# Optimization experiments

Measured on AMD Instinct MI355X. Metric: run time of the kernel, lower is better.

## Reference

```python
import jax, jax.numpy as jnp
import numpy as np

N_NODES = 100000


def _gcn_layer(x, W, b, src, dst, edge_weight):
    # GCNConv with normalize=False: linear transform, then weighted scatter-add
    h = x @ W                                   # [N, out]
    msg = h[src] * edge_weight[:, None]         # gather source features, scale per edge
    agg = jax.ops.segment_sum(msg, dst, num_segments=N_NODES)  # scatter-add to destinations
    return agg + b


def setup_inputs() -> dict:
    key = jax.random.key(0)
    k = jax.random.split(key, 6)
    N, F_in, H, C, E = N_NODES, 256, 16, 40, 3200000
    x = jax.random.normal(k[0], (N, F_in), dtype=jnp.float32)
    edge_index = jax.random.randint(k[1], (2, E), 0, N, dtype=jnp.int64)
    edge_weight = jax.random.uniform(k[2], (E,), dtype=jnp.float32)
    # Glorot-style init for weights
    W1 = jax.random.normal(k[3], (F_in, H), dtype=jnp.float32) * (1.0 / np.sqrt(F_in))
    b1 = jnp.zeros((H,), dtype=jnp.float32)
    W2 = jax.random.normal(k[4], (H, C), dtype=jnp.float32) * (1.0 / np.sqrt(H))
    b2 = jnp.zeros((C,), dtype=jnp.float32)
    return {"x": x, "edge_index": edge_index, "edge_weight": edge_weight,
            "W1": W1, "b1": b1, "W2": W2, "b2": b2}


def reference(x, edge_index, edge_weight, W1, b1, W2, b2):
    src, dst = edge_index[0], edge_index[1]
    h = jax.nn.relu(_gcn_layer(x, W1, b1, src, dst, edge_weight))
    # dropout is identity in eval mode
    h = _gcn_layer(h, W2, b2, src, dst, edge_weight)
    return jax.nn.log_softmax(h, axis=1)
```

## Files before the change

### kernel.cpp

```cpp
#include <hip/hip_runtime.h>
#include <hip/hip_bf16.h>
#include <cstdint>

#define F_IN 256
#define F_H  16
#define F_P  8
#define F_C  40

__global__ __launch_bounds__(256) void gemm1_kernel(
    const float* __restrict__ x, const float* __restrict__ W1,
    __hip_bfloat162* __restrict__ t1, int N) {
  __shared__ float wlds[F_IN * F_H];
  __shared__ float xlds[16 * 260];
  const int tid = threadIdx.x;
  const int nodeBase = blockIdx.x * 16;

  for (int i = tid; i < F_IN * F_H; i += 256) wlds[i] = W1[i];

  const float4* x4 = reinterpret_cast<const float4*>(x) + (size_t)nodeBase * (F_IN / 4);
  for (int i = tid; i < 16 * (F_IN / 4); i += 256) {
    int r = i >> 6;
    int c4 = i & 63;
    float4 v = make_float4(0.f, 0.f, 0.f, 0.f);
    if (nodeBase + r < N) v = x4[(size_t)r * (F_IN / 4) + c4];
    *reinterpret_cast<float4*>(&xlds[r * 260 + c4 * 4]) = v;
  }
  __syncthreads();

  const int r = tid >> 4;
  const int f = tid & 15;
  const float* xr = &xlds[r * 260];
  float acc = 0.f;
#pragma unroll 8
  for (int k = 0; k < F_IN; ++k) acc = fmaf(xr[k], wlds[k * F_H + f], acc);

  float hi = __shfl_down(acc, 1);
  if (((f & 1) == 0) && (nodeBase + r < N)) {
    __hip_bfloat162 h2 = __halves2bfloat162(__float2bfloat16(acc), __float2bfloat16(hi));
    t1[(size_t)(nodeBase + r) * F_P + (f >> 1)] = h2;
  }
}

__global__ __launch_bounds__(256) void scatter1_kernel(
    const __hip_bfloat162* __restrict__ t1, const int* __restrict__ ei,
    const float* __restrict__ ew, __hip_bfloat162* __restrict__ agg1,
    int N, int E) {
  int gid = blockIdx.x * 256 + threadIdx.x;
  int e = gid >> 3;
  int p = gid & 7;
  if (e >= E) return;
  int s = ei[e];
  int d = ei[E + e];
  if ((unsigned)s >= (unsigned)N || (unsigned)d >= (unsigned)N) return;
  float w = ew[e];
  __hip_bfloat162 tv = t1[(size_t)s * F_P + p];
  __hip_bfloat162 v = __halves2bfloat162(
      __float2bfloat16(__bfloat162float(tv.x) * w),
      __float2bfloat16(__bfloat162float(tv.y) * w));
  unsafeAtomicAdd(&agg1[(size_t)d * F_P + p], v);
}

__global__ __launch_bounds__(256) void scatter2_kernel(
    const __hip_bfloat162* __restrict__ agg1, const float* __restrict__ b1,
    const int* __restrict__ ei, const float* __restrict__ ew,
    __hip_bfloat162* __restrict__ agg2, int N, int E) {
  int gid = blockIdx.x * 256 + threadIdx.x;
  int e = gid >> 3;
  int p = gid & 7;
  if (e >= E) return;
  int s = ei[e];
  int d = ei[E + e];
  if ((unsigned)s >= (unsigned)N || (unsigned)d >= (unsigned)N) return;
  float w = ew[e];
  __hip_bfloat162 av = agg1[(size_t)s * F_P + p];
  float lo = __bfloat162float(av.x) + b1[2 * p];
  float hi = __bfloat162float(av.y) + b1[2 * p + 1];
  lo = lo > 0.f ? lo * w : 0.f;
  hi = hi > 0.f ? hi * w : 0.f;
  __hip_bfloat162 v = __halves2bfloat162(__float2bfloat16(lo), __float2bfloat16(hi));
  unsafeAtomicAdd(&agg2[(size_t)d * F_P + p], v);
}

__global__ __launch_bounds__(320) void gemm2_lsm_kernel(
    const __hip_bfloat162* __restrict__ agg2, const float* __restrict__ W2,
    const float* __restrict__ b2, float* __restrict__ out, int N) {
  __shared__ float w2lds[F_H * F_C];
  __shared__ float alds[8 * F_H];
  __shared__ float slds[8 * F_C];
  __shared__ float mlog[8];
  const int tid = threadIdx.x;
  const int nodeBase = blockIdx.x * 8;

  for (int i = tid; i < F_H * F_C; i += 320) w2lds[i] = W2[i];
  if (tid < 8 * F_P) {
    int node = nodeBase + (tid >> 3);
    __hip_bfloat162 v{};
    if (node < N) v = agg2[(size_t)nodeBase * F_P + tid];
    int r = tid >> 3, p = tid & 7;
    alds[r * F_H + 2 * p]     = __bfloat162float(v.x);
    alds[r * F_H + 2 * p + 1] = __bfloat162float(v.y);
  }
  __syncthreads();

  const int ln = tid / F_C;
  const int c = tid - ln * F_C;
  float acc = b2[c];
#pragma unroll
  for (int k = 0; k < F_H; ++k) acc = fmaf(alds[ln * F_H + k], w2lds[k * F_C + c], acc);
  slds[tid] = acc;
  __syncthreads();

  if (tid < 8) {
    const float* row = &slds[tid * F_C];
    float m = -INFINITY;
#pragma unroll
    for (int f = 0; f < F_C; ++f) m = fmaxf(m, row[f]);
    float s = 0.f;
#pragma unroll
    for (int f = 0; f < F_C; ++f) s += expf(row[f] - m);
    mlog[tid] = m + logf(s);
  }
  __syncthreads();

  const int node = nodeBase + ln;
  if (node < N) out[(size_t)nodeBase * F_C + tid] = slds[tid] - mlog[ln];
}

extern "C" void kernel_launch(void* const* d_in, const int* in_sizes, int n_in,
                              void* d_out, int out_size, void* d_ws, size_t ws_size,
                              hipStream_t stream) {
  const float* x  = (const float*)d_in[0];
  const int*   ei = (const int*)d_in[1];
  const float* ew = (const float*)d_in[2];
  const float* W1 = (const float*)d_in[3];
  const float* b1 = (const float*)d_in[4];
  const float* W2 = (const float*)d_in[5];
  const float* b2 = (const float*)d_in[6];
  float* out = (float*)d_out;

  const int N = in_sizes[0] / F_IN;
  const int E = in_sizes[2];

  __hip_bfloat162* t1   = (__hip_bfloat162*)d_ws;
  __hip_bfloat162* agg1 = t1 + (size_t)N * F_P;
  __hip_bfloat162* agg2 = agg1 + (size_t)N * F_P;

  hipMemsetAsync(agg1, 0, (size_t)N * F_P * 2 * sizeof(__hip_bfloat162), stream);

  gemm1_kernel<<<(N + 15) / 16, 256, 0, stream>>>(x, W1, t1, N);
  scatter1_kernel<<<((size_t)E * F_P + 255) / 256, 256, 0, stream>>>(t1, ei, ew, agg1, N, E);
  scatter2_kernel<<<((size_t)E * F_P + 255) / 256, 256, 0, stream>>>(agg1, b1, ei, ew, agg2, N, E);
  gemm2_lsm_kernel<<<(N + 7) / 8, 320, 0, stream>>>(agg2, W2, b2, out, N);
}
```

Measured before the change: 552.9 us.

## Split atomic targets, fuse zeroing into persistent GEMM1, shuffle-based log-softmax

GEMM1 becomes a persistent grid-stride kernel that reads x straight from global memory, processes four nodes per thread against a transposed W1 held in LDS, and zeroes the aggregation buffers itself, which removes the separate memset. Both scatters send edges to two accumulator copies by edge parity, meant to halve atomic contention per address; consumers add the two copies back together. GEMM2 handles 32 nodes per block, each thread computing 5 classes, and does the log-softmax reduction with width-8 shuffles and fast exp/log in place of LDS passes and extra barriers. This costs twice the accumulator memory, an extra gather per edge in scatter2, and uncoalesced x reads in GEMM1.

```diff
diff --git a/kernel.cpp b/kernel.cpp
--- a/kernel.cpp
+++ b/kernel.cpp
@@ -6,45 +6,84 @@
 #define F_H  16
 #define F_P  8
 #define F_C  40
+#define GB   512
+#define XS   32
 
 __global__ __launch_bounds__(256) void gemm1_kernel(
     const float* __restrict__ x, const float* __restrict__ W1,
-    __hip_bfloat162* __restrict__ t1, int N) {
-  __shared__ float wlds[F_IN * F_H];
-  __shared__ float xlds[16 * 260];
+    unsigned* __restrict__ t1, uint4* __restrict__ aggz, int N) {
+  __shared__ float wlds[F_H * 260];
   const int tid = threadIdx.x;
-  const int nodeBase = blockIdx.x * 16;
-
-  for (int i = tid; i < F_IN * F_H; i += 256) wlds[i] = W1[i];
-
-  const float4* x4 = reinterpret_cast<const float4*>(x) + (size_t)nodeBase * (F_IN / 4);
-  for (int i = tid; i < 16 * (F_IN / 4); i += 256) {
-    int r = i >> 6;
-    int c4 = i & 63;
-    float4 v = make_float4(0.f, 0.f, 0.f, 0.f);
-    if (nodeBase + r < N) v = x4[(size_t)r * (F_IN / 4) + c4];
-    *reinterpret_cast<float4*>(&xlds[r * 260 + c4 * 4]) = v;
+
+  {
+    const size_t tot = (size_t)N * F_P;
+    for (size_t i = blockIdx.x * 256 + tid; i < tot; i += (size_t)GB * 256)
+      aggz[i] = make_uint4(0u, 0u, 0u, 0u);
+  }
+
+  for (int i = tid; i < F_IN * F_H; i += 256) {
+    int k = i >> 4, f = i & 15;
+    wlds[f * 260 + k] = W1[i];
   }
   __syncthreads();
 
-  const int r = tid >> 4;
-  const int f = tid & 15;
-  const float* xr = &xlds[r * 260];
-  float acc = 0.f;
+  const int lane = tid & 63;
+  const int wv   = tid >> 6;
+  const int f    = lane & 15;
+  const int qs   = lane >> 4;
+  const float4* wf4 = reinterpret_cast<const float4*>(&wlds[f * 260]);
+  const float4* x4  = reinterpret_cast<const float4*>(x);
+
+  for (int nb = blockIdx.x * 64 + wv * 16 + qs * 4; nb < N; nb += GB * 64) {
+    int n0 = nb, n1 = nb + 1, n2 = nb + 2, n3 = nb + 3;
+    int c1 = n1 < N ? n1 : N - 1;
+    int c2 = n2 < N ? n2 : N - 1;
+    int c3 = n3 < N ? n3 : N - 1;
+    const float4* xr0 = x4 + (size_t)n0 * 64;
+    const float4* xr1 = x4 + (size_t)c1 * 64;
+    const float4* xr2 = x4 + (size_t)c2 * 64;
+    const float4* xr3 = x4 + (size_t)c3 * 64;
+    float a0 = 0.f, a1 = 0.f, a2 = 0.f, a3 = 0.f;
 #pragma unroll 8
-  for (int k = 0; k < F_IN; ++k) acc = fmaf(xr[k], wlds[k * F_H + f], acc);
-
-  float hi = __shfl_down(acc, 1);
-  if (((f & 1) == 0) && (nodeBase + r < N)) {
-    __hip_bfloat162 h2 = __halves2bfloat162(__float2bfloat16(acc), __float2bfloat16(hi));
-    t1[(size_t)(nodeBase + r) * F_P + (f >> 1)] = h2;
+    for (int k4 = 0; k4 < 64; ++k4) {
+      float4 w = wf4[k4];
+      float4 v0 = xr0[k4], v1 = xr1[k4], v2 = xr2[k4], v3 = xr3[k4];
+      a0 = fmaf(v0.x, w.x, a0); a0 = fmaf(v0.y, w.y, a0);
+      a0 = fmaf(v0.z, w.z, a0); a0 = fmaf(v0.w, w.w, a0);
+      a1 = fmaf(v1.x, w.x, a1); a1 = fmaf(v1.y, w.y, a1);
+      a1 = fmaf(v1.z, w.z, a1); a1 = fmaf(v1.w, w.w, a1);
+      a2 = fmaf(v2.x, w.x, a2); a2 = fmaf(v2.y, w.y, a2);
+      a2 = fmaf(v2.z, w.z, a2); a2 = fmaf(v2.w, w.w, a2);
+      a3 = fmaf(v3.x, w.x, a3); a3 = fmaf(v3.y, w.y, a3);
+      a3 = fmaf(v3.z, w.z, a3); a3 = fmaf(v3.w, w.w, a3);
+    }
+    float p0 = __shfl_xor(a0, 1), p1 = __shfl_xor(a1, 1);
+    float p2 = __shfl_xor(a2, 1), p3 = __shfl_xor(a3, 1);
+    if ((f & 1) == 0) {
+      int pp = f >> 1;
+      __hip_bfloat162 h;
+      h = __halves2bfloat162(__float2bfloat16(a0), __float2bfloat16(p0));
+      t1[(size_t)n0 * F_P + pp] = *reinterpret_cast<unsigned*>(&h);
+      if (n1 < N) {
+        h = __halves2bfloat162(__float2bfloat16(a1), __float2bfloat16(p1));
+        t1[(size_t)n1 * F_P + pp] = *reinterpret_cast<unsigned*>(&h);
+      }
+      if (n2 < N) {
+        h = __halves2bfloat162(__float2bfloat16(a2), __float2bfloat16(p2));
+        t1[(size_t)n2 * F_P + pp] = *reinterpret_cast<unsigned*>(&h);
+      }
+      if (n3 < N) {
+        h = __halves2bfloat162(__float2bfloat16(a3), __float2bfloat16(p3));
+        t1[(size_t)n3 * F_P + pp] = *reinterpret_cast<unsigned*>(&h);
+      }
+    }
   }
 }
 
 __global__ __launch_bounds__(256) void scatter1_kernel(
     const __hip_bfloat162* __restrict__ t1, const int* __restrict__ ei,
-    const float* __restrict__ ew, __hip_bfloat162* __restrict__ agg1,
-    int N, int E) {
+    const float* __restrict__ ew, __hip_bfloat162* __restrict__ agg1a,
+    __hip_bfloat162* __restrict__ agg1b, int N, int E) {
   int gid = blockIdx.x * 256 + threadIdx.x;
   int e = gid >> 3;
   int p = gid & 7;
@@ -57,13 +96,16 @@
   __hip_bfloat162 v = __halves2bfloat162(
       __float2bfloat16(__bfloat162float(tv.x) * w),
       __float2bfloat16(__bfloat162float(tv.y) * w));
-  unsafeAtomicAdd(&agg1[(size_t)d * F_P + p], v);
+  __hip_bfloat162* tgt = (e & 1) ? agg1b : agg1a;
+  unsafeAtomicAdd(&tgt[(size_t)d * F_P + p], v);
 }
 
 __global__ __launch_bounds__(256) void scatter2_kernel(
-    const __hip_bfloat162* __restrict__ agg1, const float* __restrict__ b1,
+    const __hip_bfloat162* __restrict__ agg1a,
+    const __hip_bfloat162* __restrict__ agg1b, const float* __restrict__ b1,
     const int* __restrict__ ei, const float* __restrict__ ew,
-    __hip_bfloat162* __restrict__ agg2, int N, int E) {
+    __hip_bfloat162* __restrict__ agg2a, __hip_bfloat162* __restrict__ agg2b,
+    int N, int E) {
   int gid = blockIdx.x * 256 + threadIdx.x;
   int e = gid >> 3;
   int p = gid & 7;
@@ -72,58 +114,76 @@
   int d = ei[E + e];
   if ((unsigned)s >= (unsigned)N || (unsigned)d >= (unsigned)N) return;
   float w = ew[e];
-  __hip_bfloat162 av = agg1[(size_t)s * F_P + p];
-  float lo = __bfloat162float(av.x) + b1[2 * p];
-  float hi = __bfloat162float(av.y) + b1[2 * p + 1];
-  lo = lo > 0.f ? lo * w : 0.f;
-  hi = hi > 0.f ? hi * w : 0.f;
+  float2 bb = reinterpret_cast<const float2*>(b1)[p];
+  __hip_bfloat162 va = agg1a[(size_t)s * F_P + p];
+  __hip_bfloat162 vb = agg1b[(size_t)s * F_P + p];
+  float lo = fmaxf(__bfloat162float(va.x) + __bfloat162float(vb.x) + bb.x, 0.f) * w;
+  float hi = fmaxf(__bfloat162float(va.y) + __bfloat162float(vb.y) + bb.y, 0.f) * w;
   __hip_bfloat162 v = __halves2bfloat162(__float2bfloat16(lo), __float2bfloat16(hi));
-  unsafeAtomicAdd(&agg2[(size_t)d * F_P + p], v);
-}
-
-__global__ __launch_bounds__(320) void gemm2_lsm_kernel(
-    const __hip_bfloat162* __restrict__ agg2, const float* __restrict__ W2,
+  __hip_bfloat162* tgt = (e & 1) ? agg2b : agg2a;
+  unsafeAtomicAdd(&tgt[(size_t)d * F_P + p], v);
+}
+
+__global__ __launch_bounds__(256) void gemm2_lsm_kernel(
+    const __hip_bfloat162* __restrict__ agg2a,
+    const __hip_bfloat162* __restrict__ agg2b, const float* __restrict__ W2,
     const float* __restrict__ b2, float* __restrict__ out, int N) {
   __shared__ float w2lds[F_H * F_C];
-  __shared__ float alds[8 * F_H];
-  __shared__ float slds[8 * F_C];
-  __shared__ float mlog[8];
+  __shared__ float b2lds[F_C];
+  __shared__ float alds[XS * F_H];
   const int tid = threadIdx.x;
-  const int nodeBase = blockIdx.x * 8;
-
-  for (int i = tid; i < F_H * F_C; i += 320) w2lds[i] = W2[i];
-  if (tid < 8 * F_P) {
+  const int nodeBase = blockIdx.x * XS;
+
+  for (int i = tid; i < F_H * F_C; i += 256) w2lds[i] = W2[i];
+  if (tid < F_C) b2lds[tid] = b2[tid];
+  {
     int node = nodeBase + (tid >> 3);
-    __hip_bfloat162 v{};
-    if (node < N) v = agg2[(size_t)nodeBase * F_P + tid];
-    int r = tid >> 3, p = tid & 7;
-    alds[r * F_H + 2 * p]     = __bfloat162float(v.x);
-    alds[r * F_H + 2 * p + 1] = __bfloat162float(v.y);
+    float lo = 0.f, hi = 0.f;
+    if (node < N) {
+      size_t idx = (size_t)node * F_P + (tid & 7);
+      __hip_bfloat162 va = agg2a[idx];
+      __hip_bfloat162 vb = agg2b[idx];
+      lo = __bfloat162float(va.x) + __bfloat162float(vb.x);
+      hi = __bfloat162float(va.y) + __bfloat162float(vb.y);
+    }
+    alds[(tid >> 3) * F_H + 2 * (tid & 7)]     = lo;
+    alds[(tid >> 3) * F_H + 2 * (tid & 7) + 1] = hi;
   }
   __syncthreads();
 
-  const int ln = tid / F_C;
-  const int c = tid - ln * F_C;
-  float acc = b2[c];
-#pragma unroll
-  for (int k = 0; k < F_H; ++k) acc = fmaf(alds[ln * F_H + k], w2lds[k * F_C + c], acc);
-  slds[tid] = acc;
-  __syncthreads();
-
-  if (tid < 8) {
-    const float* row = &slds[tid * F_C];
-    float m = -INFINITY;
-#pragma unroll
-    for (int f = 0; f < F_C; ++f) m = fmaxf(m, row[f]);
-    float s = 0.f;
-#pragma unroll
-    for (int f = 0; f < F_C; ++f) s += expf(row[f] - m);
-    mlog[tid] = m + logf(s);
-  }
-  __syncthreads();
-
-  const int node = nodeBase + ln;
-  if (node < N) out[(size_t)nodeBase * F_C + tid] = slds[tid] - mlog[ln];
+  const int r = tid >> 3;
+  const int l = tid & 7;
+  const int node = nodeBase + r;
+  const float* arow = &alds[r * F_H];
+
+  float acc[5];
+#pragma unroll
+  for (int j = 0; j < 5; ++j) {
+    int c = l * 5 + j;
+    float a = b2lds[c];
+#pragma unroll
+    for (int k = 0; k < F_H; ++k) a = fmaf(arow[k], w2lds[k * F_C + c], a);
+    acc[j] = a;
+  }
+
+  float m = acc[0];
+#pragma unroll
+  for (int j = 1; j < 5; ++j) m = fmaxf(m, acc[j]);
+#pragma unroll
+  for (int off = 1; off < 8; off <<= 1) m = fmaxf(m, __shfl_xor(m, off, 8));
+
+  float s = 0.f;
+#pragma unroll
+  for (int j = 0; j < 5; ++j) s += __expf(acc[j] - m);
+#pragma unroll
+  for (int off = 1; off < 8; off <<= 1) s += __shfl_xor(s, off, 8);
+
+  float ml = m + __logf(s);
+  if (node < N) {
+#pragma unroll
+    for (int j = 0; j < 5; ++j)
+      out[(size_t)node * F_C + l * 5 + j] = acc[j] - ml;
+  }
 }
 
 extern "C" void kernel_launch(void* const* d_in, const int* in_sizes, int n_in,
@@ -141,14 +201,17 @@
   const int N = in_sizes[0] / F_IN;
   const int E = in_sizes[2];
 
-  __hip_bfloat162* t1   = (__hip_bfloat162*)d_ws;
-  __hip_bfloat162* agg1 = t1 + (size_t)N * F_P;
-  __hip_bfloat162* agg2 = agg1 + (size_t)N * F_P;
-
-  hipMemsetAsync(agg1, 0, (size_t)N * F_P * 2 * sizeof(__hip_bfloat162), stream);
-
-  gemm1_kernel<<<(N + 15) / 16, 256, 0, stream>>>(x, W1, t1, N);
-  scatter1_kernel<<<((size_t)E * F_P + 255) / 256, 256, 0, stream>>>(t1, ei, ew, agg1, N, E);
-  scatter2_kernel<<<((size_t)E * F_P + 255) / 256, 256, 0, stream>>>(agg1, b1, ei, ew, agg2, N, E);
-  gemm2_lsm_kernel<<<(N + 7) / 8, 320, 0, stream>>>(agg2, W2, b2, out, N);
-}
+  __hip_bfloat162* t1    = (__hip_bfloat162*)d_ws;
+  __hip_bfloat162* agg1a = t1 + (size_t)N * F_P;
+  __hip_bfloat162* agg1b = agg1a + (size_t)N * F_P;
+  __hip_bfloat162* agg2a = agg1b + (size_t)N * F_P;
+  __hip_bfloat162* agg2b = agg2a + (size_t)N * F_P;
+
+  gemm1_kernel<<<GB, 256, 0, stream>>>(x, W1, (unsigned*)t1, (uint4*)agg1a, N);
+  scatter1_kernel<<<((size_t)E * F_P + 255) / 256, 256, 0, stream>>>(
+      t1, ei, ew, agg1a, agg1b, N, E);
+  scatter2_kernel<<<((size_t)E * F_P + 255) / 256, 256, 0, stream>>>(
+      agg1a, agg1b, b1, ei, ew, agg2a, agg2b, N, E);
+  gemm2_lsm_kernel<<<(N + XS - 1) / XS, 256, 0, stream>>>(
+      agg2a, agg2b, W2, b2, out, N);
+}
```

Result: no change. 553.6 us (+0.1%).
